# Optimization experiments

Hardware: AMD Instinct MI355X
Metric: run time of the kernel (lower is better)

The kernel has to match this reference:

```python
import jax, jax.numpy as jnp
import numpy as np

B, S, H, NH = 8, 2048, 128, 4
HS = H // NH
EPS = 1e-8


def setup_inputs() -> dict:
    key = jax.random.key(0)
    ks = jax.random.split(key, 20)
    sc = 1.0 / np.sqrt(H)
    d = {
        'item_embeds': jax.random.normal(ks[0], (B, S, H), jnp.float32),
        'behavior_embeds': jax.random.normal(ks[1], (B, S, H), jnp.float32),
        'attn_mask': jnp.zeros((B, 1, S, S), jnp.float32),
    }
    names = ['Wq', 'Wk', 'Wv', 'Wqb', 'Wkb', 'Wvb', 'Wf']
    for i, n in enumerate(names):
        d[n] = jax.random.normal(ks[2 + i], (H, H), jnp.float32) * sc
        d['b' + n[1:]] = jnp.zeros((H,), jnp.float32)
    d['ln_w'] = jnp.ones((H,), jnp.float32)
    d['ln_b'] = jnp.zeros((H,), jnp.float32)
    return d


def _split_heads(x):
    # [B,S,H] -> [B,NH,S,HS]
    return x.reshape(B, S, NH, HS).transpose(0, 2, 1, 3)


def _layer_norm(x, w, b):
    u = jnp.mean(x, -1, keepdims=True)
    s = jnp.mean((x - u) ** 2, -1, keepdims=True)
    return w * ((x - u) / jnp.sqrt(s + EPS)) + b


def reference(item_embeds, behavior_embeds, attn_mask,
              Wq, bq, Wk, bk, Wv, bv,
              Wqb, bqb, Wkb, bkb, Wvb, bvb,
              Wf, bf, ln_w, ln_b):
    Q = _split_heads(item_embeds @ Wq + bq)
    K = _split_heads(item_embeds @ Wk + bk)
    V = _split_heads(item_embeds @ Wv + bv)
    Qb = _split_heads(behavior_embeds @ Wqb + bqb)
    Kb = _split_heads(behavior_embeds @ Wkb + bkb)
    # V_behavior computed in the original forward but unused downstream
    _Vb = _split_heads(behavior_embeds @ Wvb + bvb)
    scores = (jnp.einsum('bhqd,bhkd->bhqk', Q, K)
              + jnp.einsum('bhqd,bhkd->bhqk', Qb, Kb)) / np.sqrt(HS)
    scores = scores + attn_mask
    probs = jax.nn.softmax(scores, axis=-1)
    attn_out = jnp.einsum('bhqk,bhkd->bhqd', probs, V)
    attn_out = attn_out.transpose(0, 2, 1, 3).reshape(B, S, H)
    out = attn_out @ Wf + bf
    return _layer_norm(out + item_embeds, ln_w, ln_b)
```

## Files before the change

### kernel.cpp

```cpp
#include <hip/hip_runtime.h>
#include <math.h>

typedef unsigned short ushort_t;
typedef __attribute__((ext_vector_type(8))) short bf16x8;
typedef __attribute__((ext_vector_type(4))) float f32x4;

namespace {
constexpr int B = 8, S = 2048, H = 128, NH = 4, HS = 32;
constexpr float EPS = 1e-8f;
constexpr float SCALE = 0.17677669529663687f;
constexpr int QT = 16, KT = 64;
constexpr int NE = B * S * H;
constexpr int NML = B * NH * S;
}

__device__ __forceinline__ ushort_t f2bf(float f) {
  unsigned u = __float_as_uint(f);
  unsigned r = (u + 0x7FFFu + ((u >> 16) & 1u)) >> 16;
  return (ushort_t)r;
}

__device__ __forceinline__ float bf2f(ushort_t u) {
  return __uint_as_float((unsigned)u << 16);
}

__device__ __forceinline__ f32x4 mfma16(bf16x8 a, bf16x8 b, f32x4 c) {
  return __builtin_amdgcn_mfma_f32_16x16x32_bf16(a, b, c, 0, 0, 0);
}

__global__ __launch_bounds__(256) void wcvt_kernel(
    const float* __restrict__ Wq, const float* __restrict__ Wk, const float* __restrict__ Wv,
    const float* __restrict__ Wqb, const float* __restrict__ Wkb, const float* __restrict__ Wf,
    ushort_t* __restrict__ Wt)
{
  const float* Ws[6] = {Wq, Wk, Wv, Wqb, Wkb, Wf};
  const float scl[6] = {SCALE, 1.f, 1.f, SCALE, 1.f, 1.f};
  const int m = blockIdx.y;
  const int kb = blockIdx.x;
  const float* W = Ws[m];
  const float sc = scl[m];
  __shared__ float T[32 * 132];
  const int t = threadIdx.x;
#pragma unroll
  for (int u = 0; u < 4; ++u) {
    const int idx = u * 256 + t;
    const int row = idx >> 5, c4 = idx & 31;
    const float4 v = *(const float4*)&W[(kb * 32 + row) * H + c4 * 4];
    *(float4*)&T[row * 132 + c4 * 4] = v;
  }
  __syncthreads();
#pragma unroll
  for (int u = 0; u < 16; ++u) {
    const int idx = u * 256 + t;
    const int n = idx >> 5, kk = idx & 31;
    Wt[m * (H * H) + n * H + kb * 32 + kk] = f2bf(T[kk * 132 + n] * sc);
  }
}

__global__ __launch_bounds__(256) void proj_kernel(
    const float* __restrict__ item, const float* __restrict__ beh,
    const ushort_t* __restrict__ Wt,
    const float* __restrict__ bq, const float* __restrict__ bk, const float* __restrict__ bv,
    const float* __restrict__ bqb, const float* __restrict__ bkb,
    ushort_t* __restrict__ Qo, ushort_t* __restrict__ Ko, ushort_t* __restrict__ Qbo,
    ushort_t* __restrict__ Kbo, ushort_t* __restrict__ Vto)
{
  __shared__ ushort_t Xs[32 * 136];
  __shared__ ushort_t Yb[32 * 136];
  const int t = threadIdx.x;
  const int p = blockIdx.y;
  const long r0 = (long)blockIdx.x * 32;
  const float* X = (p < 3) ? item : beh;
#pragma unroll
  for (int u = 0; u < 4; ++u) {
    const int idx = u * 256 + t;
    const int row = idx >> 5, c4 = idx & 31;
    const float4 v = *(const float4*)&X[(r0 + row) * H + c4 * 4];
    unsigned long long pk = (unsigned long long)f2bf(v.x) | ((unsigned long long)f2bf(v.y) << 16)
        | ((unsigned long long)f2bf(v.z) << 32) | ((unsigned long long)f2bf(v.w) << 48);
    *(unsigned long long*)&Xs[row * 136 + c4 * 4] = pk;
  }
  __syncthreads();

  const int w = t >> 6, l = t & 63, l15 = l & 15, quad = l >> 4;
  const int bb = (int)(r0 >> 11);
  const int s0 = (int)(r0 & (S - 1));
  const float* bias[5] = {bq, bk, bv, bqb, bkb};
  const float bscale[5] = {SCALE, 1.f, 1.f, SCALE, 1.f};
  ushort_t* dsts[5] = {Qo, Ko, Vto, Qbo, Kbo};

  bf16x8 af[2][4];
#pragma unroll
  for (int mt = 0; mt < 2; ++mt)
#pragma unroll
    for (int ks = 0; ks < 4; ++ks)
      af[mt][ks] = *(const bf16x8*)&Xs[(mt * 16 + l15) * 136 + ks * 32 + quad * 8];

  f32x4 acc[2][2];
#pragma unroll
  for (int nt = 0; nt < 2; ++nt) {
    const float bcol = bias[p][w * 32 + nt * 16 + l15] * bscale[p];
#pragma unroll
    for (int mt = 0; mt < 2; ++mt)
      acc[mt][nt] = (f32x4){bcol, bcol, bcol, bcol};
  }
  const ushort_t* Wp = Wt + p * (H * H);
#pragma unroll
  for (int ks = 0; ks < 4; ++ks) {
    bf16x8 bfr[2];
#pragma unroll
    for (int nt = 0; nt < 2; ++nt)
      bfr[nt] = *(const bf16x8*)&Wp[(w * 32 + nt * 16 + l15) * H + ks * 32 + quad * 8];
#pragma unroll
    for (int mt = 0; mt < 2; ++mt)
#pragma unroll
      for (int nt = 0; nt < 2; ++nt)
        acc[mt][nt] = mfma16(af[mt][ks], bfr[nt], acc[mt][nt]);
  }
#pragma unroll
  for (int mt = 0; mt < 2; ++mt)
#pragma unroll
    for (int nt = 0; nt < 2; ++nt)
#pragma unroll
      for (int r = 0; r < 4; ++r)
        Yb[(mt * 16 + quad * 4 + r) * 136 + w * 32 + nt * 16 + l15] = f2bf(acc[mt][nt][r]);
  __syncthreads();
  ushort_t* dst = dsts[p];
  if (p == 2) {
    const int d = t >> 1, sh = (t & 1) * 16;
    ushort_t tmp[16];
#pragma unroll
    for (int i = 0; i < 16; ++i) tmp[i] = Yb[(sh + i) * 136 + d];
    const long gidx = ((long)(bb * NH + (d >> 5)) * HS + (d & 31)) * S + s0 + sh;
    *(uint4*)&dst[gidx] = *(const uint4*)&tmp[0];
    *(uint4*)&dst[gidx + 8] = *(const uint4*)&tmp[8];
  } else {
    const int row = t >> 3, cb = (t & 7) * 16;
    const int h = cb >> 5, dd = cb & 31;
    const long gidx = ((long)(bb * NH + h) * S + s0 + row) * HS + dd;
    *(uint4*)&dst[gidx] = *(const uint4*)&Yb[row * 136 + cb];
    *(uint4*)&dst[gidx + 8] = *(const uint4*)&Yb[row * 136 + cb + 8];
  }
}

__global__ __launch_bounds__(256, 2) void attn_kernel(
    const ushort_t* __restrict__ Q, const ushort_t* __restrict__ K,
    const ushort_t* __restrict__ Qb, const ushort_t* __restrict__ Kb,
    const ushort_t* __restrict__ Vt, const float* __restrict__ mask,
    ushort_t* __restrict__ Op, float* __restrict__ Mp, float* __restrict__ Lp)
{
  __shared__ ushort_t Pb[NH][2][16 * 72];
  const int t = threadIdx.x;
  const int w = t >> 6;
  const int l = t & 63, l15 = l & 15, quad = l >> 4, quad4 = quad * 4;
  const int q0 = blockIdx.x * 32;
  const int b = blockIdx.y;
  const int half_ = blockIdx.z;
  const long hQ = (long)(b * NH + w) * S * HS;
  const long hV = (long)(b * NH + w) * HS * S;
  const ushort_t* Kp  = K + hQ;
  const ushort_t* Kbp = Kb + hQ;
  const ushort_t* Vp  = Vt + hV;

  bf16x8 qf[2], qbf[2];
#pragma unroll
  for (int c = 0; c < 2; ++c) {
    qf[c]  = *(const bf16x8*)&Q[hQ + (long)(q0 + c * 16 + l15) * HS + quad * 8];
    qbf[c] = *(const bf16x8*)&Qb[hQ + (long)(q0 + c * 16 + l15) * HS + quad * 8];
  }

  const float* mrow[2][4];
#pragma unroll
  for (int c = 0; c < 2; ++c)
#pragma unroll
    for (int r = 0; r < 4; ++r)
      mrow[c][r] = mask + ((long)b * S + q0 + c * 16 + quad4 + r) * S + l15;

  float mold[2][4], lsum[2][4];
  f32x4 O[2][2];
#pragma unroll
  for (int c = 0; c < 2; ++c) {
#pragma unroll
    for (int r = 0; r < 4; ++r) { mold[c][r] = -1e30f; lsum[c][r] = 0.f; }
#pragma unroll
    for (int dt = 0; dt < 2; ++dt) O[c][dt] = (f32x4){0.f, 0.f, 0.f, 0.f};
  }

  const int kt0 = half_ * (S / KT / 2), kt1 = kt0 + (S / KT / 2);

  f32x4 scA[2][4], scB[2][4];
#pragma unroll
  for (int c = 0; c < 2; ++c)
#pragma unroll
    for (int nt = 0; nt < 4; ++nt)
#pragma unroll
      for (int r = 0; r < 4; ++r)
        scA[c][nt][r] = mrow[c][r][kt0 * KT + nt * 16];

  auto body = [&](f32x4 (&sc)[2][4], f32x4 (&scn)[2][4], int k0, int k0n, bool pre) {
    bf16x8 kf[4], kbf[4];
#pragma unroll
    for (int nt = 0; nt < 4; ++nt) {
      kf[nt]  = *(const bf16x8*)&Kp[(long)(k0 + nt * 16 + l15) * HS + quad * 8];
      kbf[nt] = *(const bf16x8*)&Kbp[(long)(k0 + nt * 16 + l15) * HS + quad * 8];
    }
    bf16x8 vf[2][2];
#pragma unroll
    for (int dt = 0; dt < 2; ++dt)
#pragma unroll
      for (int ks = 0; ks < 2; ++ks)
        vf[dt][ks] = *(const bf16x8*)&Vp[(long)(dt * 16 + l15) * S + k0 + ks * 32 + quad * 8];
    if (pre) {
#pragma unroll
      for (int c = 0; c < 2; ++c)
#pragma unroll
        for (int nt = 0; nt < 4; ++nt)
#pragma unroll
          for (int r = 0; r < 4; ++r)
            scn[c][nt][r] = mrow[c][r][k0n + nt * 16];
    }
#pragma unroll
    for (int c = 0; c < 2; ++c)
#pragma unroll
      for (int nt = 0; nt < 4; ++nt) {
        sc[c][nt] = mfma16(qbf[c], kbf[nt], sc[c][nt]);
        sc[c][nt] = mfma16(qf[c], kf[nt], sc[c][nt]);
      }
    bool grow = false;
#pragma unroll
    for (int c = 0; c < 2; ++c)
#pragma unroll
      for (int r = 0; r < 4; ++r) {
        const float gm = fmaxf(fmaxf(sc[c][0][r], sc[c][1][r]),
                               fmaxf(sc[c][2][r], sc[c][3][r]));
        grow = grow || (gm > mold[c][r] + 8.f);
      }
    if (__any(grow)) {
#pragma unroll
      for (int c = 0; c < 2; ++c) {
        float alpha[4];
#pragma unroll
        for (int r = 0; r < 4; ++r) {
          float rm = fmaxf(fmaxf(sc[c][0][r], sc[c][1][r]),
                           fmaxf(sc[c][2][r], sc[c][3][r]));
          rm = fmaxf(rm, __shfl_xor(rm, 1));
          rm = fmaxf(rm, __shfl_xor(rm, 2));
          rm = fmaxf(rm, __shfl_xor(rm, 4));
          rm = fmaxf(rm, __shfl_xor(rm, 8));
          const float mnew = fmaxf(mold[c][r], rm);
          alpha[r] = __expf(mold[c][r] - mnew);
          lsum[c][r] *= alpha[r];
          mold[c][r] = mnew;
        }
#pragma unroll
        for (int dt = 0; dt < 2; ++dt)
#pragma unroll
          for (int r = 0; r < 4; ++r)
            O[c][dt][r] *= alpha[r];
      }
    }
#pragma unroll
    for (int c = 0; c < 2; ++c) {
#pragma unroll
      for (int r = 0; r < 4; ++r) {
        float rs = 0.f;
#pragma unroll
        for (int nt = 0; nt < 4; ++nt) {
          const float p = __expf(sc[c][nt][r] - mold[c][r]);
          sc[c][nt][r] = p;
          rs += p;
        }
        lsum[c][r] += rs;
      }
      ushort_t* Pw = Pb[w][c];
#pragma unroll
      for (int nt = 0; nt < 4; ++nt)
#pragma unroll
        for (int r = 0; r < 4; ++r)
          Pw[(quad4 + r) * 72 + nt * 16 + l15] = f2bf(sc[c][nt][r]);
    }
#pragma unroll
    for (int c = 0; c < 2; ++c) {
      const ushort_t* Pw = Pb[w][c];
      bf16x8 pf[2];
#pragma unroll
      for (int ks = 0; ks < 2; ++ks)
        pf[ks] = *(const bf16x8*)&Pw[l15 * 72 + ks * 32 + quad * 8];
#pragma unroll
      for (int dt = 0; dt < 2; ++dt)
#pragma unroll
        for (int ks = 0; ks < 2; ++ks)
          O[c][dt] = mfma16(pf[ks], vf[dt][ks], O[c][dt]);
    }
  };

  for (int kt = kt0; kt < kt1; kt += 2) {
    body(scA, scB, kt * KT, (kt + 1) * KT, true);
    body(scB, scA, (kt + 1) * KT, (kt + 2) * KT, kt + 2 < kt1);
  }

#pragma unroll
  for (int c = 0; c < 2; ++c)
#pragma unroll
    for (int r = 0; r < 4; ++r) {
      float s = lsum[c][r];
      s += __shfl_xor(s, 1);
      s += __shfl_xor(s, 2);
      s += __shfl_xor(s, 4);
      s += __shfl_xor(s, 8);
      lsum[c][r] = s;
    }
#pragma unroll
  for (int c = 0; c < 2; ++c) {
#pragma unroll
    for (int r = 0; r < 4; ++r) {
      const float inv = 1.f / lsum[c][r];
      const long row = (long)b * S + q0 + c * 16 + quad4 + r;
#pragma unroll
      for (int dt = 0; dt < 2; ++dt)
        Op[(long)half_ * NE + row * H + w * 32 + dt * 16 + l15] = f2bf(O[c][dt][r] * inv);
    }
    if (l15 == 0) {
#pragma unroll
      for (int r = 0; r < 4; ++r) {
        const long idx = ((long)(half_ * B + b) * NH + w) * S + q0 + c * 16 + quad4 + r;
        Mp[idx] = mold[c][r];
        Lp[idx] = lsum[c][r];
      }
    }
  }
}

__global__ __launch_bounds__(256) void out_kernel(
    const ushort_t* __restrict__ Op, const float* __restrict__ Mp, const float* __restrict__ Lp,
    const float* __restrict__ item,
    const ushort_t* __restrict__ Wft, const float* __restrict__ bf_,
    const float* __restrict__ lnw, const float* __restrict__ lnb,
    float* __restrict__ out)
{
  __shared__ ushort_t As[16 * 136];
  __shared__ float Ys[16 * 132];
  const int t = threadIdx.x;
  const long r0 = (long)blockIdx.x * 16;
  {
    const int row = t >> 4, c8 = t & 15;
    const long g = r0 + row;
    const int bb = (int)(g >> 11);
    const int ss = (int)(g & (S - 1));
    const int col0 = c8 * 8;
    const int h = col0 >> 5;
    const long mlidx = ((long)bb * NH + h) * S + ss;
    const float m1 = Mp[mlidx], m2 = Mp[(long)NML + mlidx];
    const float l1 = Lp[mlidx], l2 = Lp[(long)NML + mlidx];
    const float M = fmaxf(m1, m2);
    const float w1 = l1 * __expf(m1 - M), w2 = l2 * __expf(m2 - M);
    const float inv = 1.f / (w1 + w2);
    const float wa = w1 * inv, wb = w2 * inv;
    const uint4 a1 = *(const uint4*)&Op[g * H + col0];
    const uint4 a2 = *(const uint4*)&Op[(long)NE + g * H + col0];
    const ushort_t* p1 = (const ushort_t*)&a1;
    const ushort_t* p2 = (const ushort_t*)&a2;
    ushort_t mg[8];
#pragma unroll
    for (int i = 0; i < 8; ++i)
      mg[i] = f2bf(bf2f(p1[i]) * wa + bf2f(p2[i]) * wb);
    *(uint4*)&As[row * 136 + col0] = *(const uint4*)&mg[0];
  }
  __syncthreads();
  const int w = t >> 6, l = t & 63, l15 = l & 15, quad = l >> 4;
  f32x4 acc[2];
#pragma unroll
  for (int nt = 0; nt < 2; ++nt) {
    const float bcol = bf_[w * 32 + nt * 16 + l15];
    acc[nt] = (f32x4){bcol, bcol, bcol, bcol};
  }
#pragma unroll
  for (int ks = 0; ks < 4; ++ks) {
    const bf16x8 a = *(const bf16x8*)&As[l15 * 136 + ks * 32 + quad * 8];
#pragma unroll
    for (int nt = 0; nt < 2; ++nt) {
      const bf16x8 bfr = *(const bf16x8*)&Wft[(w * 32 + nt * 16 + l15) * H + ks * 32 + quad * 8];
      acc[nt] = mfma16(a, bfr, acc[nt]);
    }
  }
#pragma unroll
  for (int nt = 0; nt < 2; ++nt)
#pragma unroll
    for (int r = 0; r < 4; ++r) {
      const int rl = quad * 4 + r;
      const int col = w * 32 + nt * 16 + l15;
      Ys[rl * 132 + col] = acc[nt][r] + item[(r0 + rl) * H + col];
    }
  __syncthreads();
  const int rl = t >> 4, ch = t & 15;
  float v[8];
#pragma unroll
  for (int g = 0; g < 2; ++g) {
    const float4 y = *(const float4*)&Ys[rl * 132 + ch * 8 + g * 4];
    v[g * 4 + 0] = y.x; v[g * 4 + 1] = y.y; v[g * 4 + 2] = y.z; v[g * 4 + 3] = y.w;
  }
  float s = 0.f;
#pragma unroll
  for (int i = 0; i < 8; ++i) s += v[i];
  s += __shfl_xor(s, 1);
  s += __shfl_xor(s, 2);
  s += __shfl_xor(s, 4);
  s += __shfl_xor(s, 8);
  const float u_ = s * (1.f / H);
  float s2 = 0.f;
#pragma unroll
  for (int i = 0; i < 8; ++i) { const float d = v[i] - u_; s2 += d * d; }
  s2 += __shfl_xor(s2, 1);
  s2 += __shfl_xor(s2, 2);
  s2 += __shfl_xor(s2, 4);
  s2 += __shfl_xor(s2, 8);
  const float rinv = rsqrtf(s2 * (1.f / H) + EPS);
#pragma unroll
  for (int g = 0; g < 2; ++g) {
    float4 o;
    const int col = ch * 8 + g * 4;
    o.x = lnw[col + 0] * ((v[g * 4 + 0] - u_) * rinv) + lnb[col + 0];
    o.y = lnw[col + 1] * ((v[g * 4 + 1] - u_) * rinv) + lnb[col + 1];
    o.z = lnw[col + 2] * ((v[g * 4 + 2] - u_) * rinv) + lnb[col + 2];
    o.w = lnw[col + 3] * ((v[g * 4 + 3] - u_) * rinv) + lnb[col + 3];
    *(float4*)&out[(r0 + rl) * H + col] = o;
  }
}

extern "C" void kernel_launch(void* const* d_in, const int* in_sizes, int n_in,
                              void* d_out, int out_size, void* d_ws, size_t ws_size,
                              hipStream_t stream) {
  const float* item = (const float*)d_in[0];
  const float* beh  = (const float*)d_in[1];
  const float* mask = (const float*)d_in[2];
  const float* Wq  = (const float*)d_in[3];  const float* bq  = (const float*)d_in[4];
  const float* Wk  = (const float*)d_in[5];  const float* bk  = (const float*)d_in[6];
  const float* Wv  = (const float*)d_in[7];  const float* bv  = (const float*)d_in[8];
  const float* Wqb = (const float*)d_in[9];  const float* bqb = (const float*)d_in[10];
  const float* Wkb = (const float*)d_in[11]; const float* bkb = (const float*)d_in[12];
  const float* Wf  = (const float*)d_in[15]; const float* bfv = (const float*)d_in[16];
  const float* lnw = (const float*)d_in[17]; const float* lnb = (const float*)d_in[18];
  float* out = (float*)d_out;

  ushort_t* ws = (ushort_t*)d_ws;
  ushort_t* Qw   = ws;
  ushort_t* Kw   = Qw + NE;
  ushort_t* Qbw  = Kw + NE;
  ushort_t* Kbw  = Qbw + NE;
  ushort_t* Vtw  = Kbw + NE;
  ushort_t* Opw  = Vtw + NE;
  ushort_t* Wt   = Opw + 2 * (long)NE;
  float* Mpw = (float*)(Wt + 6 * H * H);
  float* Lpw = Mpw + 2 * (long)NML;

  wcvt_kernel<<<dim3(4, 6), 256, 0, stream>>>(Wq, Wk, Wv, Wqb, Wkb, Wf, Wt);
  proj_kernel<<<dim3((B * S) / 32, 5), 256, 0, stream>>>(
      item, beh, Wt, bq, bk, bv, bqb, bkb, Qw, Kw, Qbw, Kbw, Vtw);
  attn_kernel<<<dim3(S / 32, B, 2), 256, 0, stream>>>(
      Qw, Kw, Qbw, Kbw, Vtw, mask, Opw, Mpw, Lpw);
  out_kernel<<<dim3((B * S) / 16), 256, 0, stream>>>(
      Opw, Mpw, Lpw, item, Wt + 5 * H * H, bfv, lnw, lnb, out);
}
```

Before: 328.8 us.

## Remove split-K attention and write normalized output directly

```diff
diff --git a/kernel.cpp b/kernel.cpp
--- a/kernel.cpp
+++ b/kernel.cpp
@@ -11,17 +11,12 @@
 constexpr float SCALE = 0.17677669529663687f;
 constexpr int QT = 16, KT = 64;
 constexpr int NE = B * S * H;
-constexpr int NML = B * NH * S;
 }
 
 __device__ __forceinline__ ushort_t f2bf(float f) {
   unsigned u = __float_as_uint(f);
   unsigned r = (u + 0x7FFFu + ((u >> 16) & 1u)) >> 16;
   return (ushort_t)r;
-}
-
-__device__ __forceinline__ float bf2f(ushort_t u) {
-  return __uint_as_float((unsigned)u << 16);
 }
 
 __device__ __forceinline__ f32x4 mfma16(bf16x8 a, bf16x8 b, f32x4 c) {
@@ -147,7 +142,7 @@
     const ushort_t* __restrict__ Q, const ushort_t* __restrict__ K,
     const ushort_t* __restrict__ Qb, const ushort_t* __restrict__ Kb,
     const ushort_t* __restrict__ Vt, const float* __restrict__ mask,
-    ushort_t* __restrict__ Op, float* __restrict__ Mp, float* __restrict__ Lp)
+    ushort_t* __restrict__ attn_out)
 {
   __shared__ ushort_t Pb[NH][2][16 * 72];
   const int t = threadIdx.x;
@@ -155,7 +150,6 @@
   const int l = t & 63, l15 = l & 15, quad = l >> 4, quad4 = quad * 4;
   const int q0 = blockIdx.x * 32;
   const int b = blockIdx.y;
-  const int half_ = blockIdx.z;
   const long hQ = (long)(b * NH + w) * S * HS;
   const long hV = (long)(b * NH + w) * HS * S;
   const ushort_t* Kp  = K + hQ;
@@ -186,8 +180,6 @@
     for (int dt = 0; dt < 2; ++dt) O[c][dt] = (f32x4){0.f, 0.f, 0.f, 0.f};
   }
 
-  const int kt0 = half_ * (S / KT / 2), kt1 = kt0 + (S / KT / 2);
-
   f32x4 scA[2][4], scB[2][4];
 #pragma unroll
   for (int c = 0; c < 2; ++c)
@@ -195,7 +187,7 @@
     for (int nt = 0; nt < 4; ++nt)
 #pragma unroll
       for (int r = 0; r < 4; ++r)
-        scA[c][nt][r] = mrow[c][r][kt0 * KT + nt * 16];
+        scA[c][nt][r] = mrow[c][r][nt * 16];
 
   auto body = [&](f32x4 (&sc)[2][4], f32x4 (&scn)[2][4], int k0, int k0n, bool pre) {
     bf16x8 kf[4], kbf[4];
@@ -294,9 +286,9 @@
     }
   };
 
-  for (int kt = kt0; kt < kt1; kt += 2) {
+  for (int kt = 0; kt < S / KT; kt += 2) {
     body(scA, scB, kt * KT, (kt + 1) * KT, true);
-    body(scB, scA, (kt + 1) * KT, (kt + 2) * KT, kt + 2 < kt1);
+    body(scB, scA, (kt + 1) * KT, (kt + 2) * KT, kt + 2 < S / KT);
   }
 
 #pragma unroll
@@ -311,29 +303,19 @@
       lsum[c][r] = s;
     }
 #pragma unroll
-  for (int c = 0; c < 2; ++c) {
+  for (int c = 0; c < 2; ++c)
 #pragma unroll
     for (int r = 0; r < 4; ++r) {
       const float inv = 1.f / lsum[c][r];
       const long row = (long)b * S + q0 + c * 16 + quad4 + r;
 #pragma unroll
       for (int dt = 0; dt < 2; ++dt)
-        Op[(long)half_ * NE + row * H + w * 32 + dt * 16 + l15] = f2bf(O[c][dt][r] * inv);
-    }
-    if (l15 == 0) {
-#pragma unroll
-      for (int r = 0; r < 4; ++r) {
-        const long idx = ((long)(half_ * B + b) * NH + w) * S + q0 + c * 16 + quad4 + r;
-        Mp[idx] = mold[c][r];
-        Lp[idx] = lsum[c][r];
-      }
-    }
-  }
+        attn_out[row * H + w * 32 + dt * 16 + l15] = f2bf(O[c][dt][r] * inv);
+    }
 }
 
 __global__ __launch_bounds__(256) void out_kernel(
-    const ushort_t* __restrict__ Op, const float* __restrict__ Mp, const float* __restrict__ Lp,
-    const float* __restrict__ item,
+    const ushort_t* __restrict__ attn, const float* __restrict__ item,
     const ushort_t* __restrict__ Wft, const float* __restrict__ bf_,
     const float* __restrict__ lnw, const float* __restrict__ lnb,
     float* __restrict__ out)
@@ -344,27 +326,7 @@
   const long r0 = (long)blockIdx.x * 16;
   {
     const int row = t >> 4, c8 = t & 15;
-    const long g = r0 + row;
-    const int bb = (int)(g >> 11);
-    const int ss = (int)(g & (S - 1));
-    const int col0 = c8 * 8;
-    const int h = col0 >> 5;
-    const long mlidx = ((long)bb * NH + h) * S + ss;
-    const float m1 = Mp[mlidx], m2 = Mp[(long)NML + mlidx];
-    const float l1 = Lp[mlidx], l2 = Lp[(long)NML + mlidx];
-    const float M = fmaxf(m1, m2);
-    const float w1 = l1 * __expf(m1 - M), w2 = l2 * __expf(m2 - M);
-    const float inv = 1.f / (w1 + w2);
-    const float wa = w1 * inv, wb = w2 * inv;
-    const uint4 a1 = *(const uint4*)&Op[g * H + col0];
-    const uint4 a2 = *(const uint4*)&Op[(long)NE + g * H + col0];
-    const ushort_t* p1 = (const ushort_t*)&a1;
-    const ushort_t* p2 = (const ushort_t*)&a2;
-    ushort_t mg[8];
-#pragma unroll
-    for (int i = 0; i < 8; ++i)
-      mg[i] = f2bf(bf2f(p1[i]) * wa + bf2f(p2[i]) * wb);
-    *(uint4*)&As[row * 136 + col0] = *(const uint4*)&mg[0];
+    *(uint4*)&As[row * 136 + c8 * 8] = *(const uint4*)&attn[(r0 + row) * H + c8 * 8];
   }
   __syncthreads();
   const int w = t >> 6, l = t & 63, l15 = l & 15, quad = l >> 4;
@@ -448,16 +410,14 @@
   ushort_t* Qbw  = Kw + NE;
   ushort_t* Kbw  = Qbw + NE;
   ushort_t* Vtw  = Kbw + NE;
-  ushort_t* Opw  = Vtw + NE;
-  ushort_t* Wt   = Opw + 2 * (long)NE;
-  float* Mpw = (float*)(Wt + 6 * H * H);
-  float* Lpw = Mpw + 2 * (long)NML;
+  ushort_t* Attw = Vtw + NE;
+  ushort_t* Wt   = Attw + NE;
 
   wcvt_kernel<<<dim3(4, 6), 256, 0, stream>>>(Wq, Wk, Wv, Wqb, Wkb, Wf, Wt);
   proj_kernel<<<dim3((B * S) / 32, 5), 256, 0, stream>>>(
       item, beh, Wt, bq, bk, bv, bqb, bkb, Qw, Kw, Qbw, Kbw, Vtw);
-  attn_kernel<<<dim3(S / 32, B, 2), 256, 0, stream>>>(
-      Qw, Kw, Qbw, Kbw, Vtw, mask, Opw, Mpw, Lpw);
+  attn_kernel<<<dim3(S / 32, B), 256, 0, stream>>>(
+      Qw, Kw, Qbw, Kbw, Vtw, mask, Attw);
   out_kernel<<<dim3((B * S) / 16), 256, 0, stream>>>(
-      Opw, Mpw, Lpw, item, Wt + 5 * H * H, bfv, lnw, lnb, out);
-}
+      Attw, item, Wt + 5 * H * H, bfv, lnw, lnb, out);
+}
```

Measured after the change: 322.4 us. About the same (-2.0%).
